# Performance work log

Hardware: AMD Instinct MI355X
Metric: run time of the kernel (lower is better)

## Reference

```python
import jax, jax.numpy as jnp
import numpy as np

NP_, B_ = 44, 400000

def setup_inputs() -> dict:
    key = jax.random.key(0)
    k_x, k1, k2, k3, k4 = jax.random.split(key, 5)
    return {
        "X": jax.random.normal(k_x, (NP_, 1, B_), dtype=jnp.float32),
        "lin1s": jax.random.normal(k1, (NP_, 4, 1), dtype=jnp.float32),
        "lin2s": jax.random.normal(k2, (NP_, 8, 4), dtype=jnp.float32),
        "lin3s": jax.random.normal(k3, (NP_, 4, 8), dtype=jnp.float32),
        "lin4s": jax.random.normal(k4, (NP_, 1, 4), dtype=jnp.float32),
    }

def reference(X, lin1s, lin2s, lin3s, lin4s):
    # forward_all: chained batched tiny GEMMs with ReLU, 'lik,lkj->lij'
    h = jax.nn.relu(jnp.einsum('lik,lkj->lij', lin1s, X))   # (NP, 4, B)
    h = jax.nn.relu(jnp.einsum('lik,lkj->lij', lin2s, h))   # (NP, 8, B)
    h = jax.nn.relu(jnp.einsum('lik,lkj->lij', lin3s, h))   # (NP, 4, B)
    return jnp.einsum('lik,lkj->lij', lin4s, h)             # (NP, 1, B)
```

## Files before the change

### kernel.cpp

```cpp
#include <hip/hip_runtime.h>

#define NP 44
#define B  400000
#define B4 (B / 4)
#define BLK 256

__global__ __launch_bounds__(BLK) void fused_mlp_kernel(
    const float* __restrict__ X,
    const float* __restrict__ W1,
    const float* __restrict__ W2,
    const float* __restrict__ W3,
    const float* __restrict__ W4,
    float* __restrict__ out)
{
    const int l   = blockIdx.y;
    const int idx = blockIdx.x * BLK + threadIdx.x;
    if (idx >= B4) return;

    const float* p1 = W1 + l * 4;
    const float* p2 = W2 + l * 32;
    const float* p3 = W3 + l * 32;
    const float* p4 = W4 + l * 4;

    float w1[4], w2[8][4], w3[4][8], w4[4];
#pragma unroll
    for (int i = 0; i < 4; ++i) w1[i] = p1[i];
#pragma unroll
    for (int i = 0; i < 8; ++i)
#pragma unroll
        for (int k = 0; k < 4; ++k) w2[i][k] = p2[i * 4 + k];
#pragma unroll
    for (int i = 0; i < 4; ++i)
#pragma unroll
        for (int k = 0; k < 8; ++k) w3[i][k] = p3[i * 8 + k];
#pragma unroll
    for (int i = 0; i < 4; ++i) w4[i] = p4[i];

    const float4* Xp = (const float4*)(X + (size_t)l * B);
    float4*       Op = (float4*)(out + (size_t)l * B);

    float4 xv = Xp[idx];
    float xs[4] = {xv.x, xv.y, xv.z, xv.w};
    float res[4];

#pragma unroll
    for (int e = 0; e < 4; ++e) {
        const float x = xs[e];

        float h1[4];
#pragma unroll
        for (int i = 0; i < 4; ++i) h1[i] = fmaxf(w1[i] * x, 0.0f);

        float h2[8];
#pragma unroll
        for (int i = 0; i < 8; ++i) {
            float a = 0.0f;
#pragma unroll
            for (int k = 0; k < 4; ++k) a = fmaf(w2[i][k], h1[k], a);
            h2[i] = fmaxf(a, 0.0f);
        }

        float h3[4];
#pragma unroll
        for (int i = 0; i < 4; ++i) {
            float a = 0.0f;
#pragma unroll
            for (int k = 0; k < 8; ++k) a = fmaf(w3[i][k], h2[k], a);
            h3[i] = fmaxf(a, 0.0f);
        }

        float a = 0.0f;
#pragma unroll
        for (int k = 0; k < 4; ++k) a = fmaf(w4[k], h3[k], a);
        res[e] = a;
    }

    Op[idx] = make_float4(res[0], res[1], res[2], res[3]);
}

extern "C" void kernel_launch(void* const* d_in, const int* in_sizes, int n_in,
                              void* d_out, int out_size, void* d_ws, size_t ws_size,
                              hipStream_t stream) {
    const float* X  = (const float*)d_in[0];
    const float* W1 = (const float*)d_in[1];
    const float* W2 = (const float*)d_in[2];
    const float* W3 = (const float*)d_in[3];
    const float* W4 = (const float*)d_in[4];
    float* out = (float*)d_out;

    dim3 grid((B4 + BLK - 1) / BLK, NP);
    fused_mlp_kernel<<<grid, BLK, 0, stream>>>(X, W1, W2, W3, W4, out);
}
```

Measured before the change: 144.1 us.

## Use packed float2 math and process four float4 chunks per thread

Rewrites the per-element MLP to run on 2-wide float vectors so the compiler can emit packed FP32 FMA/max instructions. It also makes each thread handle four float4 chunks strided by the block size, which amortises the per-thread weight loads and issues several independent global loads up front. Blocks that lie entirely inside the range take a fast path with no bounds checks, and the last block uses a guarded path. The cost is higher register pressure and a quarter as many blocks.

```diff
diff --git a/kernel.cpp b/kernel.cpp
--- a/kernel.cpp
+++ b/kernel.cpp
@@ -1,9 +1,49 @@
 #include <hip/hip_runtime.h>
 
-#define NP 44
-#define B  400000
-#define B4 (B / 4)
+#define NP  44
+#define B   400000
+#define B4  (B / 4)
 #define BLK 256
+#define CPT 4
+
+typedef float v2f __attribute__((ext_vector_type(2)));
+
+__device__ __forceinline__ v2f relu2(v2f a) {
+    return __builtin_elementwise_max(a, (v2f)0.0f);
+}
+
+__device__ __forceinline__ v2f mlp_pair(
+    const float w1[4], const float w2[8][4],
+    const float w3[4][8], const float w4[4], v2f x)
+{
+#pragma clang fp contract(fast)
+    v2f h1[4];
+#pragma unroll
+    for (int i = 0; i < 4; ++i) h1[i] = relu2(w1[i] * x);
+
+    v2f h2[8];
+#pragma unroll
+    for (int i = 0; i < 8; ++i) {
+        v2f a = w2[i][0] * h1[0];
+#pragma unroll
+        for (int k = 1; k < 4; ++k) a += w2[i][k] * h1[k];
+        h2[i] = relu2(a);
+    }
+
+    v2f h3[4];
+#pragma unroll
+    for (int i = 0; i < 4; ++i) {
+        v2f a = w3[i][0] * h2[0];
+#pragma unroll
+        for (int k = 1; k < 8; ++k) a += w3[i][k] * h2[k];
+        h3[i] = relu2(a);
+    }
+
+    v2f a = w4[0] * h3[0];
+#pragma unroll
+    for (int k = 1; k < 4; ++k) a += w4[k] * h3[k];
+    return a;
+}
 
 __global__ __launch_bounds__(BLK) void fused_mlp_kernel(
     const float* __restrict__ X,
@@ -13,9 +53,8 @@
     const float* __restrict__ W4,
     float* __restrict__ out)
 {
-    const int l   = blockIdx.y;
-    const int idx = blockIdx.x * BLK + threadIdx.x;
-    if (idx >= B4) return;
+    const int l    = blockIdx.y;
+    const int base = blockIdx.x * (BLK * CPT) + threadIdx.x;
 
     const float* p1 = W1 + l * 4;
     const float* p2 = W2 + l * 32;
@@ -39,43 +78,36 @@
     const float4* Xp = (const float4*)(X + (size_t)l * B);
     float4*       Op = (float4*)(out + (size_t)l * B);
 
-    float4 xv = Xp[idx];
-    float xs[4] = {xv.x, xv.y, xv.z, xv.w};
-    float res[4];
+    if ((blockIdx.x + 1) * (BLK * CPT) <= B4) {
+        float4 xv[CPT];
+#pragma unroll
+        for (int c = 0; c < CPT; ++c) xv[c] = Xp[base + c * BLK];
 
+        float4 rv[CPT];
 #pragma unroll
-    for (int e = 0; e < 4; ++e) {
-        const float x = xs[e];
-
-        float h1[4];
+        for (int c = 0; c < CPT; ++c) {
+            v2f p0 = {xv[c].x, xv[c].y};
+            v2f p1v = {xv[c].z, xv[c].w};
+            v2f r0 = mlp_pair(w1, w2, w3, w4, p0);
+            v2f r1 = mlp_pair(w1, w2, w3, w4, p1v);
+            rv[c] = make_float4(r0.x, r0.y, r1.x, r1.y);
+        }
 #pragma unroll
-        for (int i = 0; i < 4; ++i) h1[i] = fmaxf(w1[i] * x, 0.0f);
-
-        float h2[8];
+        for (int c = 0; c < CPT; ++c) Op[base + c * BLK] = rv[c];
+    } else {
 #pragma unroll
-        for (int i = 0; i < 8; ++i) {
-            float a = 0.0f;
-#pragma unroll
-            for (int k = 0; k < 4; ++k) a = fmaf(w2[i][k], h1[k], a);
-            h2[i] = fmaxf(a, 0.0f);
+        for (int c = 0; c < CPT; ++c) {
+            const int idx = base + c * BLK;
+            if (idx < B4) {
+                float4 xv = Xp[idx];
+                v2f p0 = {xv.x, xv.y};
+                v2f p1v = {xv.z, xv.w};
+                v2f r0 = mlp_pair(w1, w2, w3, w4, p0);
+                v2f r1 = mlp_pair(w1, w2, w3, w4, p1v);
+                Op[idx] = make_float4(r0.x, r0.y, r1.x, r1.y);
+            }
         }
-
-        float h3[4];
-#pragma unroll
-        for (int i = 0; i < 4; ++i) {
-            float a = 0.0f;
-#pragma unroll
-            for (int k = 0; k < 8; ++k) a = fmaf(w3[i][k], h2[k], a);
-            h3[i] = fmaxf(a, 0.0f);
-        }
-
-        float a = 0.0f;
-#pragma unroll
-        for (int k = 0; k < 4; ++k) a = fmaf(w4[k], h3[k], a);
-        res[e] = a;
     }
-
-    Op[idx] = make_float4(res[0], res[1], res[2], res[3]);
 }
 
 extern "C" void kernel_launch(void* const* d_in, const int* in_sizes, int n_in,
@@ -88,6 +120,6 @@
     const float* W4 = (const float*)d_in[4];
     float* out = (float*)d_out;
 
-    dim3 grid((B4 + BLK - 1) / BLK, NP);
+    dim3 grid((B4 + BLK * CPT - 1) / (BLK * CPT), NP);
     fused_mlp_kernel<<<grid, BLK, 0, stream>>>(X, W1, W2, W3, W4, out);
 }
```

Result: slower. 147.8 us (+2.6%).
